# Kernel tuning notes

Hardware: AMD Instinct MI355X
Metric: run time of the kernel (lower is better)

## Reference

```python
import jax, jax.numpy as jnp
import numpy as np

R = 4
EPS = 0.1


def _box(x, r=R):
    # Depthwise (2r+1)x(2r+1) mean filter with 'SAME' zero padding, faithful to
    # F.conv2d(x, box_kernel, groups=C, padding='same').
    c = x.shape[1]
    k = 2 * r + 1
    kernel = jnp.full((c, 1, k, k), 1.0 / (k * k), dtype=x.dtype)  # OIHW, groups=C
    return jax.lax.conv_general_dilated(
        x, kernel, window_strides=(1, 1), padding='SAME',
        dimension_numbers=('NCHW', 'OIHW', 'NCHW'), feature_group_count=c)


def setup_inputs() -> dict:
    key = jax.random.key(0)
    k1, k2 = jax.random.split(key)
    x = jax.random.uniform(k1, (8, 3, 768, 768), dtype=jnp.float32)
    y = jax.random.uniform(k2, (8, 3, 768, 768), dtype=jnp.float32)
    return {"x": x, "y": y}


def reference(x, y):
    n, c, h, w = x.shape
    # N: box filter of an all-ones [1,1,H,W] image (edge-normalization counts)
    N = _box(jnp.ones((1, 1, h, w), dtype=x.dtype))
    mean_x = _box(x) / N
    mean_y = _box(y) / N
    cov_xy = _box(x * y) / N - mean_x * mean_y
    var_x = _box(x * x) / N - mean_x * mean_x
    A = cov_xy / (var_x + EPS)
    b = mean_y - A * mean_x
    mean_A = _box(A) / N
    mean_b = _box(b) / N
    return mean_A * x + mean_b
```

## Files before the change

### kernel.cpp

```cpp
#include <hip/hip_runtime.h>

#define H 768
#define W 768
#define SW 256
#define RW 272
#define ABW 264
#define ROWS 64
#define NSTEP 40
#define RADIUS 4

__global__ __launch_bounds__(256, 4) void gf_stream2(
    const float* __restrict__ xg, const float* __restrict__ yg,
    float* __restrict__ outg)
{
    __shared__ float2 xybuf[2][2][RW];
    __shared__ float2 abbuf[2][2][ABW];
    __shared__ float4 tring[9][8];

    const int t     = threadIdx.x;
    const int base  = blockIdx.x * SW;
    const int R0    = blockIdx.y * ROWS;
    const int plane = blockIdx.z;

    const float* xp = xg + (size_t)plane * (H * W);
    const float* yp = yg + (size_t)plane * (H * W);
    float*       op = outg + (size_t)plane * (H * W);

    const int  a_abs   = base + t - 4;
    const bool a_colok = (a_abs >= 0) && (a_abs < W);
    const float invCwA = a_colok
        ? 1.0f / (float)(min(a_abs + RADIUS, W - 1) - max(a_abs - RADIUS, 0) + 1) : 0.f;
    const int  a2_abs   = base + 252 + t;
    const bool a2_colok = (t < 8) && (a2_abs < W);
    const float invCwA2 = a2_colok
        ? 1.0f / (float)(min(a2_abs + RADIUS, W - 1) - max(a2_abs - RADIUS, 0) + 1) : 0.f;
    const int   c_abs  = base + t;
    const float invCwO = 1.0f / (float)(min(c_abs + RADIUS, W - 1) - max(c_abs - RADIUS, 0) + 1);
    const int  lc1   = base + t - 8;
    const bool lc1ok = (lc1 >= 0) && (lc1 < W);
    const int  lc2   = base + 248 + t;
    const bool lc2ok = (t < 16) && (lc2 < W);

    float hx[9], hy[9], hxy[9], hxx[9];
    float hA9[9], hB9[9];
#pragma unroll
    for (int i = 0; i < 9; ++i) { hx[i]=hy[i]=hxy[i]=hxx[i]=0.f; hA9[i]=hB9[i]=0.f; }
    float vx=0.f, vy=0.f, vxy=0.f, vxx=0.f;
    float v2x=0.f, v2y=0.f, v2xy=0.f, v2xx=0.f;
    float vA=0.f, vB=0.f;

    if (t < 72) ((float4*)tring)[t] = make_float4(0.f,0.f,0.f,0.f);

    {
        int g0 = R0 - 8, g1 = R0 - 7;
        bool k0 = (g0 >= 0), k1 = (g1 >= 0);
        const float *x0 = xp + g0 * W, *y0 = yp + g0 * W;
        const float *x1 = xp + g1 * W, *y1 = yp + g1 * W;
        float a, b;
        a = (k0 && lc1ok) ? x0[lc1] : 0.f;  b = (k0 && lc1ok) ? y0[lc1] : 0.f;
        xybuf[0][0][t] = make_float2(a, b);
        a = (k1 && lc1ok) ? x1[lc1] : 0.f;  b = (k1 && lc1ok) ? y1[lc1] : 0.f;
        xybuf[0][1][t] = make_float2(a, b);
        if (t < 16) {
            a = (k0 && lc2ok) ? x0[lc2] : 0.f;  b = (k0 && lc2ok) ? y0[lc2] : 0.f;
            xybuf[0][0][256 + t] = make_float2(a, b);
            a = (k1 && lc2ok) ? x1[lc2] : 0.f;  b = (k1 && lc2ok) ? y1[lc2] : 0.f;
            xybuf[0][1][256 + t] = make_float2(a, b);
        }
    }
    float p0x, p0y, p0x2, p0y2, p1x, p1y, p1x2, p1y2;
    {
        int g0 = R0 - 6, g1 = R0 - 5;
        bool k0 = (g0 >= 0), k1 = (g1 >= 0);
        const float *x0 = xp + g0 * W, *y0 = yp + g0 * W;
        const float *x1 = xp + g1 * W, *y1 = yp + g1 * W;
        p0x  = (k0 && lc1ok) ? x0[lc1] : 0.f;  p0y  = (k0 && lc1ok) ? y0[lc1] : 0.f;
        p1x  = (k1 && lc1ok) ? x1[lc1] : 0.f;  p1y  = (k1 && lc1ok) ? y1[lc1] : 0.f;
        p0x2 = (k0 && lc2ok) ? x0[lc2] : 0.f;  p0y2 = (k0 && lc2ok) ? y0[lc2] : 0.f;
        p1x2 = (k1 && lc2ok) ? x1[lc2] : 0.f;  p1y2 = (k1 && lc2ok) ? y1[lc2] : 0.f;
    }
    __syncthreads();

    for (int S0 = 0; S0 < NSTEP; S0 += 9) {
#pragma unroll
        for (int u = 0; u < 9; ++u) {
            const int S = S0 + u;
            if (S < NSTEP) {
                const int r0  = R0 - 16 + 2 * S;
                const int cur = S & 1, nxt = cur ^ 1;

                xybuf[nxt][0][t] = make_float2(p0x, p0y);
                xybuf[nxt][1][t] = make_float2(p1x, p1y);
                if (t < 16) {
                    xybuf[nxt][0][256 + t] = make_float2(p0x2, p0y2);
                    xybuf[nxt][1][256 + t] = make_float2(p1x2, p1y2);
                }
                {
                    int g0 = r0 + 12, g1 = r0 + 13;
                    bool k0 = (g0 >= 0) && (g0 < H);
                    bool k1 = (g1 >= 0) && (g1 < H);
                    const float *x0 = xp + g0 * W, *y0 = yp + g0 * W;
                    const float *x1 = xp + g1 * W, *y1 = yp + g1 * W;
                    p0x  = (k0 && lc1ok) ? x0[lc1] : 0.f;  p0y  = (k0 && lc1ok) ? y0[lc1] : 0.f;
                    p1x  = (k1 && lc1ok) ? x1[lc1] : 0.f;  p1y  = (k1 && lc1ok) ? y1[lc1] : 0.f;
                    p0x2 = (k0 && lc2ok) ? x0[lc2] : 0.f;  p0y2 = (k0 && lc2ok) ? y0[lc2] : 0.f;
                    p1x2 = (k1 && lc2ok) ? x1[lc2] : 0.f;  p1y2 = (k1 && lc2ok) ? y1[lc2] : 0.f;
                }
                float xq0 = (r0 >= 0)     ? xp[r0 * W + c_abs]       : 0.f;
                float xq1 = (r0 + 1 >= 0) ? xp[(r0 + 1) * W + c_abs] : 0.f;

                {
                    const int sl = (2 * u) % 9;
                    float nx=0.f, ny=0.f, nxy=0.f, nxx=0.f;
#pragma unroll
                    for (int d = 0; d < 9; ++d) {
                        float2 v = xybuf[cur][0][t + d];
                        nx += v.x; ny += v.y; nxy += v.x * v.y; nxx += v.x * v.x;
                    }
                    vx  += nx  - hx[sl];  hx[sl]  = nx;
                    vy  += ny  - hy[sl];  hy[sl]  = ny;
                    vxy += nxy - hxy[sl]; hxy[sl] = nxy;
                    vxx += nxx - hxx[sl]; hxx[sl] = nxx;

                    const int ra = r0 + 4;
                    const bool rowok = (S >= 4) && (ra >= 0) && (ra < H);
                    float Aout = 0.f, Bout = 0.f;
                    if (rowok && a_colok) {
                        const float invCh = 1.0f /
                            (float)(min(ra + RADIUS, H - 1) - max(ra - RADIUS, 0) + 1);
                        float invN = invCh * invCwA;
                        float mx = vx * invN, my = vy * invN;
                        float cov = vxy * invN - mx * my;
                        float vr  = vxx * invN - mx * mx;
                        float Ai = cov * __builtin_amdgcn_rcpf(vr + 0.1f);
                        Aout = Ai; Bout = my - Ai * mx;
                    }
                    abbuf[cur][0][t] = make_float2(Aout, Bout);
                }
                {
                    const int sl = (2 * u + 1) % 9;
                    float nx=0.f, ny=0.f, nxy=0.f, nxx=0.f;
#pragma unroll
                    for (int d = 0; d < 9; ++d) {
                        float2 v = xybuf[cur][1][t + d];
                        nx += v.x; ny += v.y; nxy += v.x * v.y; nxx += v.x * v.x;
                    }
                    vx  += nx  - hx[sl];  hx[sl]  = nx;
                    vy  += ny  - hy[sl];  hy[sl]  = ny;
                    vxy += nxy - hxy[sl]; hxy[sl] = nxy;
                    vxx += nxx - hxx[sl]; hxx[sl] = nxx;

                    const int ra = r0 + 5;
                    const bool rowok = (S >= 4) && (ra >= 0) && (ra < H);
                    float Aout = 0.f, Bout = 0.f;
                    if (rowok && a_colok) {
                        const float invCh = 1.0f /
                            (float)(min(ra + RADIUS, H - 1) - max(ra - RADIUS, 0) + 1);
                        float invN = invCh * invCwA;
                        float mx = vx * invN, my = vy * invN;
                        float cov = vxy * invN - mx * my;
                        float vr  = vxx * invN - mx * mx;
                        float Ai = cov * __builtin_amdgcn_rcpf(vr + 0.1f);
                        Aout = Ai; Bout = my - Ai * mx;
                    }
                    abbuf[cur][1][t] = make_float2(Aout, Bout);
                }
                if (t < 8) {
#pragma unroll
                    for (int j = 0; j < 2; ++j) {
                        const int sl = (2 * u + j) % 9;
                        float ex=0.f, ey=0.f, exy=0.f, exx=0.f;
#pragma unroll
                        for (int d = 0; d < 9; ++d) {
                            float2 v = xybuf[cur][j][256 + t + d];
                            ex += v.x; ey += v.y; exy += v.x * v.y; exx += v.x * v.x;
                        }
                        float4 old = tring[sl][t];
                        v2x += ex - old.x; v2y += ey - old.y;
                        v2xy += exy - old.z; v2xx += exx - old.w;
                        tring[sl][t] = make_float4(ex, ey, exy, exx);

                        const int ra = r0 + 4 + j;
                        const bool rowok = (S >= 4) && (ra >= 0) && (ra < H);
                        float A2 = 0.f, B2 = 0.f;
                        if (rowok && a2_colok) {
                            const float invCh = 1.0f /
                                (float)(min(ra + RADIUS, H - 1) - max(ra - RADIUS, 0) + 1);
                            float invN = invCh * invCwA2;
                            float mx = v2x * invN, my = v2y * invN;
                            float cov = v2xy * invN - mx * my;
                            float vr  = v2xx * invN - mx * mx;
                            float Ai = cov * __builtin_amdgcn_rcpf(vr + 0.1f);
                            A2 = Ai; B2 = my - Ai * mx;
                        }
                        abbuf[cur][j][256 + t] = make_float2(A2, B2);
                    }
                }

                __syncthreads();

                {
                    const int sl = (2 * u) % 9;
                    float hA=0.f, hB=0.f;
#pragma unroll
                    for (int d = 0; d < 9; ++d) {
                        float2 v = abbuf[cur][0][t + d];
                        hA += v.x; hB += v.y;
                    }
                    vA += hA - hA9[sl]; hA9[sl] = hA;
                    vB += hB - hB9[sl]; hB9[sl] = hB;
                    if (S >= 8) {
                        const float invCh = 1.0f /
                            (float)(min(r0 + RADIUS, H - 1) - max(r0 - RADIUS, 0) + 1);
                        float invN = invCh * invCwO;
                        op[r0 * W + c_abs] = (vA * invN) * xq0 + (vB * invN);
                    }
                }
                {
                    const int sl = (2 * u + 1) % 9;
                    float hA=0.f, hB=0.f;
#pragma unroll
                    for (int d = 0; d < 9; ++d) {
                        float2 v = abbuf[cur][1][t + d];
                        hA += v.x; hB += v.y;
                    }
                    vA += hA - hA9[sl]; hA9[sl] = hA;
                    vB += hB - hB9[sl]; hB9[sl] = hB;
                    if (S >= 8) {
                        const int r = r0 + 1;
                        const float invCh = 1.0f /
                            (float)(min(r + RADIUS, H - 1) - max(r - RADIUS, 0) + 1);
                        float invN = invCh * invCwO;
                        op[r * W + c_abs] = (vA * invN) * xq1 + (vB * invN);
                    }
                }
            }
        }
    }
}

extern "C" void kernel_launch(void* const* d_in, const int* in_sizes, int n_in,
                              void* d_out, int out_size, void* d_ws, size_t ws_size,
                              hipStream_t stream) {
    const float* x = (const float*)d_in[0];
    const float* y = (const float*)d_in[1];
    float* out = (float*)d_out;

    dim3 grid(W / SW, H / ROWS, 24);
    dim3 block(256);
    hipLaunchKernelGGL(gf_stream2, grid, block, 0, stream, x, y, out);
}
```

Measured before the change: 103.8 us.

## Pack row pairs into float4 LDS, reuse staged x via register ring, shrink strips

Interleaves the two rows of each step into one float4 LDS buffer so every tap is a single 128-bit LDS read covering both rows, for both the xy stage and the A/B stage. The centre x value is kept in a 9-slot register delay line instead of being reloaded from global memory for the final output. The strip height drops from 64 to 48 rows and the occupancy hint rises to 5 blocks per SIMD, giving more blocks in flight at the cost of a larger share of halo rows. A/B stores and the second box pass are skipped during warm-up steps.

```diff
diff --git a/kernel.cpp b/kernel.cpp
--- a/kernel.cpp
+++ b/kernel.cpp
@@ -5,16 +5,16 @@
 #define SW 256
 #define RW 272
 #define ABW 264
-#define ROWS 64
-#define NSTEP 40
+#define ROWS 48
+#define NSTEP 32
 #define RADIUS 4
 
-__global__ __launch_bounds__(256, 4) void gf_stream2(
+__global__ __launch_bounds__(256, 5) void gf_stream3(
     const float* __restrict__ xg, const float* __restrict__ yg,
     float* __restrict__ outg)
 {
-    __shared__ float2 xybuf[2][2][RW];
-    __shared__ float2 abbuf[2][2][ABW];
+    __shared__ float4 xybuf[2][RW];
+    __shared__ float4 abbuf[2][ABW];
     __shared__ float4 tring[9][8];
 
     const int t     = threadIdx.x;
@@ -43,8 +43,9 @@
 
     float hx[9], hy[9], hxy[9], hxx[9];
     float hA9[9], hB9[9];
-#pragma unroll
-    for (int i = 0; i < 9; ++i) { hx[i]=hy[i]=hxy[i]=hxx[i]=0.f; hA9[i]=hB9[i]=0.f; }
+    float xdel[9];
+#pragma unroll
+    for (int i = 0; i < 9; ++i) { hx[i]=hy[i]=hxy[i]=hxx[i]=0.f; hA9[i]=hB9[i]=0.f; xdel[i]=0.f; }
     float vx=0.f, vy=0.f, vxy=0.f, vxx=0.f;
     float v2x=0.f, v2y=0.f, v2xy=0.f, v2xx=0.f;
     float vA=0.f, vB=0.f;
@@ -56,16 +57,13 @@
         bool k0 = (g0 >= 0), k1 = (g1 >= 0);
         const float *x0 = xp + g0 * W, *y0 = yp + g0 * W;
         const float *x1 = xp + g1 * W, *y1 = yp + g1 * W;
-        float a, b;
-        a = (k0 && lc1ok) ? x0[lc1] : 0.f;  b = (k0 && lc1ok) ? y0[lc1] : 0.f;
-        xybuf[0][0][t] = make_float2(a, b);
-        a = (k1 && lc1ok) ? x1[lc1] : 0.f;  b = (k1 && lc1ok) ? y1[lc1] : 0.f;
-        xybuf[0][1][t] = make_float2(a, b);
+        float a0 = (k0 && lc1ok) ? x0[lc1] : 0.f, b0 = (k0 && lc1ok) ? y0[lc1] : 0.f;
+        float a1 = (k1 && lc1ok) ? x1[lc1] : 0.f, b1 = (k1 && lc1ok) ? y1[lc1] : 0.f;
+        xybuf[0][t] = make_float4(a0, b0, a1, b1);
         if (t < 16) {
-            a = (k0 && lc2ok) ? x0[lc2] : 0.f;  b = (k0 && lc2ok) ? y0[lc2] : 0.f;
-            xybuf[0][0][256 + t] = make_float2(a, b);
-            a = (k1 && lc2ok) ? x1[lc2] : 0.f;  b = (k1 && lc2ok) ? y1[lc2] : 0.f;
-            xybuf[0][1][256 + t] = make_float2(a, b);
+            float c0 = (k0 && lc2ok) ? x0[lc2] : 0.f, d0 = (k0 && lc2ok) ? y0[lc2] : 0.f;
+            float c1 = (k1 && lc2ok) ? x1[lc2] : 0.f, d1 = (k1 && lc2ok) ? y1[lc2] : 0.f;
+            xybuf[0][256 + t] = make_float4(c0, d0, c1, d1);
         }
     }
     float p0x, p0y, p0x2, p0y2, p1x, p1y, p1x2, p1y2;
@@ -88,13 +86,14 @@
             if (S < NSTEP) {
                 const int r0  = R0 - 16 + 2 * S;
                 const int cur = S & 1, nxt = cur ^ 1;
-
-                xybuf[nxt][0][t] = make_float2(p0x, p0y);
-                xybuf[nxt][1][t] = make_float2(p1x, p1y);
-                if (t < 16) {
-                    xybuf[nxt][0][256 + t] = make_float2(p0x2, p0y2);
-                    xybuf[nxt][1][256 + t] = make_float2(p1x2, p1y2);
-                }
+                const int s0 = (2 * u) % 9, s1 = (2 * u + 1) % 9;
+
+                const float xq0 = xdel[(2 * u + 1) % 9];
+                const float xq1 = xdel[(2 * u + 2) % 9];
+
+                xybuf[nxt][t] = make_float4(p0x, p0y, p1x, p1y);
+                if (t < 16) xybuf[nxt][256 + t] = make_float4(p0x2, p0y2, p1x2, p1y2);
+
                 {
                     int g0 = r0 + 12, g1 = r0 + 13;
                     bool k0 = (g0 >= 0) && (g0 < H);
@@ -106,126 +105,112 @@
                     p0x2 = (k0 && lc2ok) ? x0[lc2] : 0.f;  p0y2 = (k0 && lc2ok) ? y0[lc2] : 0.f;
                     p1x2 = (k1 && lc2ok) ? x1[lc2] : 0.f;  p1y2 = (k1 && lc2ok) ? y1[lc2] : 0.f;
                 }
-                float xq0 = (r0 >= 0)     ? xp[r0 * W + c_abs]       : 0.f;
-                float xq1 = (r0 + 1 >= 0) ? xp[(r0 + 1) * W + c_abs] : 0.f;
-
-                {
-                    const int sl = (2 * u) % 9;
-                    float nx=0.f, ny=0.f, nxy=0.f, nxx=0.f;
+
+                float nx0=0.f,ny0=0.f,nxy0=0.f,nxx0=0.f;
+                float nx1=0.f,ny1=0.f,nxy1=0.f,nxx1=0.f;
+                float4 tap;
+#pragma unroll
+                for (int d = 0; d < 9; ++d) {
+                    tap = xybuf[cur][t + d];
+                    nx0 += tap.x; ny0 += tap.y; nxy0 += tap.x * tap.y; nxx0 += tap.x * tap.x;
+                    nx1 += tap.z; ny1 += tap.w; nxy1 += tap.z * tap.w; nxx1 += tap.z * tap.z;
+                }
+                xdel[s0] = tap.x;
+                xdel[s1] = tap.z;
+
+                vx  += nx0  - hx[s0];  hx[s0]  = nx0;
+                vy  += ny0  - hy[s0];  hy[s0]  = ny0;
+                vxy += nxy0 - hxy[s0]; hxy[s0] = nxy0;
+                vxx += nxx0 - hxx[s0]; hxx[s0] = nxx0;
+                float A0 = 0.f, B0 = 0.f;
+                const int ra0 = r0 + 4;
+                if (S >= 4 && a_colok && ra0 >= 0 && ra0 < H) {
+                    const float invCh = 1.0f /
+                        (float)(min(ra0 + RADIUS, H - 1) - max(ra0 - RADIUS, 0) + 1);
+                    float invN = invCh * invCwA;
+                    float mx = vx * invN, my = vy * invN;
+                    float cov = vxy * invN - mx * my;
+                    float vr  = vxx * invN - mx * mx;
+                    A0 = cov * __builtin_amdgcn_rcpf(vr + 0.1f);
+                    B0 = my - A0 * mx;
+                }
+                vx  += nx1  - hx[s1];  hx[s1]  = nx1;
+                vy  += ny1  - hy[s1];  hy[s1]  = ny1;
+                vxy += nxy1 - hxy[s1]; hxy[s1] = nxy1;
+                vxx += nxx1 - hxx[s1]; hxx[s1] = nxx1;
+                float A1 = 0.f, B1 = 0.f;
+                const int ra1 = r0 + 5;
+                if (S >= 4 && a_colok && ra1 >= 0 && ra1 < H) {
+                    const float invCh = 1.0f /
+                        (float)(min(ra1 + RADIUS, H - 1) - max(ra1 - RADIUS, 0) + 1);
+                    float invN = invCh * invCwA;
+                    float mx = vx * invN, my = vy * invN;
+                    float cov = vxy * invN - mx * my;
+                    float vr  = vxx * invN - mx * mx;
+                    A1 = cov * __builtin_amdgcn_rcpf(vr + 0.1f);
+                    B1 = my - A1 * mx;
+                }
+                if (S >= 4) abbuf[cur][t] = make_float4(A0, B0, A1, B1);
+
+                if (t < 8) {
+                    float ex0=0.f,ey0=0.f,exy0=0.f,exx0=0.f;
+                    float ex1=0.f,ey1=0.f,exy1=0.f,exx1=0.f;
 #pragma unroll
                     for (int d = 0; d < 9; ++d) {
-                        float2 v = xybuf[cur][0][t + d];
-                        nx += v.x; ny += v.y; nxy += v.x * v.y; nxx += v.x * v.x;
-                    }
-                    vx  += nx  - hx[sl];  hx[sl]  = nx;
-                    vy  += ny  - hy[sl];  hy[sl]  = ny;
-                    vxy += nxy - hxy[sl]; hxy[sl] = nxy;
-                    vxx += nxx - hxx[sl]; hxx[sl] = nxx;
-
-                    const int ra = r0 + 4;
-                    const bool rowok = (S >= 4) && (ra >= 0) && (ra < H);
-                    float Aout = 0.f, Bout = 0.f;
-                    if (rowok && a_colok) {
-                        const float invCh = 1.0f /
-                            (float)(min(ra + RADIUS, H - 1) - max(ra - RADIUS, 0) + 1);
-                        float invN = invCh * invCwA;
-                        float mx = vx * invN, my = vy * invN;
-                        float cov = vxy * invN - mx * my;
-                        float vr  = vxx * invN - mx * mx;
-                        float Ai = cov * __builtin_amdgcn_rcpf(vr + 0.1f);
-                        Aout = Ai; Bout = my - Ai * mx;
-                    }
-                    abbuf[cur][0][t] = make_float2(Aout, Bout);
-                }
-                {
-                    const int sl = (2 * u + 1) % 9;
-                    float nx=0.f, ny=0.f, nxy=0.f, nxx=0.f;
+                        float4 v = xybuf[cur][256 + t + d];
+                        ex0 += v.x; ey0 += v.y; exy0 += v.x * v.y; exx0 += v.x * v.x;
+                        ex1 += v.z; ey1 += v.w; exy1 += v.z * v.w; exx1 += v.z * v.z;
+                    }
+                    float4 o0 = tring[s0][t];
+                    v2x += ex0 - o0.x; v2y += ey0 - o0.y; v2xy += exy0 - o0.z; v2xx += exx0 - o0.w;
+                    tring[s0][t] = make_float4(ex0, ey0, exy0, exx0);
+                    float A20 = 0.f, B20 = 0.f;
+                    if (S >= 4 && a2_colok && ra0 >= 0 && ra0 < H) {
+                        const float invCh = 1.0f /
+                            (float)(min(ra0 + RADIUS, H - 1) - max(ra0 - RADIUS, 0) + 1);
+                        float invN = invCh * invCwA2;
+                        float mx = v2x * invN, my = v2y * invN;
+                        float cov = v2xy * invN - mx * my;
+                        float vr  = v2xx * invN - mx * mx;
+                        A20 = cov * __builtin_amdgcn_rcpf(vr + 0.1f);
+                        B20 = my - A20 * mx;
+                    }
+                    float4 o1 = tring[s1][t];
+                    v2x += ex1 - o1.x; v2y += ey1 - o1.y; v2xy += exy1 - o1.z; v2xx += exx1 - o1.w;
+                    tring[s1][t] = make_float4(ex1, ey1, exy1, exx1);
+                    float A21 = 0.f, B21 = 0.f;
+                    if (S >= 4 && a2_colok && ra1 >= 0 && ra1 < H) {
+                        const float invCh = 1.0f /
+                            (float)(min(ra1 + RADIUS, H - 1) - max(ra1 - RADIUS, 0) + 1);
+                        float invN = invCh * invCwA2;
+                        float mx = v2x * invN, my = v2y * invN;
+                        float cov = v2xy * invN - mx * my;
+                        float vr  = v2xx * invN - mx * mx;
+                        A21 = cov * __builtin_amdgcn_rcpf(vr + 0.1f);
+                        B21 = my - A21 * mx;
+                    }
+                    if (S >= 4) abbuf[cur][256 + t] = make_float4(A20, B20, A21, B21);
+                }
+
+                __syncthreads();
+
+                if (S >= 4) {
+                    float hA0=0.f,hB0=0.f,hA1=0.f,hB1=0.f;
 #pragma unroll
                     for (int d = 0; d < 9; ++d) {
-                        float2 v = xybuf[cur][1][t + d];
-                        nx += v.x; ny += v.y; nxy += v.x * v.y; nxx += v.x * v.x;
-                    }
-                    vx  += nx  - hx[sl];  hx[sl]  = nx;
-                    vy  += ny  - hy[sl];  hy[sl]  = ny;
-                    vxy += nxy - hxy[sl]; hxy[sl] = nxy;
-                    vxx += nxx - hxx[sl]; hxx[sl] = nxx;
-
-                    const int ra = r0 + 5;
-                    const bool rowok = (S >= 4) && (ra >= 0) && (ra < H);
-                    float Aout = 0.f, Bout = 0.f;
-                    if (rowok && a_colok) {
-                        const float invCh = 1.0f /
-                            (float)(min(ra + RADIUS, H - 1) - max(ra - RADIUS, 0) + 1);
-                        float invN = invCh * invCwA;
-                        float mx = vx * invN, my = vy * invN;
-                        float cov = vxy * invN - mx * my;
-                        float vr  = vxx * invN - mx * mx;
-                        float Ai = cov * __builtin_amdgcn_rcpf(vr + 0.1f);
-                        Aout = Ai; Bout = my - Ai * mx;
-                    }
-                    abbuf[cur][1][t] = make_float2(Aout, Bout);
-                }
-                if (t < 8) {
-#pragma unroll
-                    for (int j = 0; j < 2; ++j) {
-                        const int sl = (2 * u + j) % 9;
-                        float ex=0.f, ey=0.f, exy=0.f, exx=0.f;
-#pragma unroll
-                        for (int d = 0; d < 9; ++d) {
-                            float2 v = xybuf[cur][j][256 + t + d];
-                            ex += v.x; ey += v.y; exy += v.x * v.y; exx += v.x * v.x;
-                        }
-                        float4 old = tring[sl][t];
-                        v2x += ex - old.x; v2y += ey - old.y;
-                        v2xy += exy - old.z; v2xx += exx - old.w;
-                        tring[sl][t] = make_float4(ex, ey, exy, exx);
-
-                        const int ra = r0 + 4 + j;
-                        const bool rowok = (S >= 4) && (ra >= 0) && (ra < H);
-                        float A2 = 0.f, B2 = 0.f;
-                        if (rowok && a2_colok) {
-                            const float invCh = 1.0f /
-                                (float)(min(ra + RADIUS, H - 1) - max(ra - RADIUS, 0) + 1);
-                            float invN = invCh * invCwA2;
-                            float mx = v2x * invN, my = v2y * invN;
-                            float cov = v2xy * invN - mx * my;
-                            float vr  = v2xx * invN - mx * mx;
-                            float Ai = cov * __builtin_amdgcn_rcpf(vr + 0.1f);
-                            A2 = Ai; B2 = my - Ai * mx;
-                        }
-                        abbuf[cur][j][256 + t] = make_float2(A2, B2);
-                    }
-                }
-
-                __syncthreads();
-
-                {
-                    const int sl = (2 * u) % 9;
-                    float hA=0.f, hB=0.f;
-#pragma unroll
-                    for (int d = 0; d < 9; ++d) {
-                        float2 v = abbuf[cur][0][t + d];
-                        hA += v.x; hB += v.y;
-                    }
-                    vA += hA - hA9[sl]; hA9[sl] = hA;
-                    vB += hB - hB9[sl]; hB9[sl] = hB;
+                        float4 v = abbuf[cur][t + d];
+                        hA0 += v.x; hB0 += v.y; hA1 += v.z; hB1 += v.w;
+                    }
+                    vA += hA0 - hA9[s0]; hA9[s0] = hA0;
+                    vB += hB0 - hB9[s0]; hB9[s0] = hB0;
                     if (S >= 8) {
                         const float invCh = 1.0f /
                             (float)(min(r0 + RADIUS, H - 1) - max(r0 - RADIUS, 0) + 1);
                         float invN = invCh * invCwO;
                         op[r0 * W + c_abs] = (vA * invN) * xq0 + (vB * invN);
                     }
-                }
-                {
-                    const int sl = (2 * u + 1) % 9;
-                    float hA=0.f, hB=0.f;
-#pragma unroll
-                    for (int d = 0; d < 9; ++d) {
-                        float2 v = abbuf[cur][1][t + d];
-                        hA += v.x; hB += v.y;
-                    }
-                    vA += hA - hA9[sl]; hA9[sl] = hA;
-                    vB += hB - hB9[sl]; hB9[sl] = hB;
+                    vA += hA1 - hA9[s1]; hA9[s1] = hA1;
+                    vB += hB1 - hB9[s1]; hB9[s1] = hB1;
                     if (S >= 8) {
                         const int r = r0 + 1;
                         const float invCh = 1.0f /
@@ -248,5 +233,5 @@
 
     dim3 grid(W / SW, H / ROWS, 24);
     dim3 block(256);
-    hipLaunchKernelGGL(gf_stream2, grid, block, 0, stream, x, y, out);
+    hipLaunchKernelGGL(gf_stream3, grid, block, 0, stream, x, y, out);
 }
```

Result: slower. 309.4 us (+198.0%).
